# Performance work log

Measured on AMD Instinct MI355X. Metric: run time of the kernel, lower is better.

Reference implementation:

```python
import jax, jax.numpy as jnp
import numpy as np

ALPHA = 1.1
COMMISSION = 0.05
BET_PCT = 0.02
B = 4_194_304
T = 6  # num traps


def setup_inputs() -> dict:
    key = jax.random.key(0)
    k1, k2, k3, k4 = jax.random.split(key, 4)
    predicted_probs = jax.random.uniform(k1, (B, T), dtype=jnp.float32)
    true_winners = (jax.random.uniform(k2, (B, T)) > 0.8).astype(jnp.float32)
    market_odds = jax.random.uniform(k3, (B, T), dtype=jnp.float32) * 10.0
    invalid = jax.random.uniform(k4, (B, 1)) < 0.1
    market_odds = jnp.where(invalid, 0.0, market_odds)
    return {"predicted_probs": predicted_probs, "true_winners": true_winners,
            "market_odds": market_odds}


def reference(predicted_probs, true_winners, market_odds):
    batch_size = predicted_probs.shape[0]
    payout_scale = BET_PCT * (1.0 - COMMISSION)

    has_valid_odds = jnp.any(market_odds > 0, axis=1)  # [B]
    # expected profit per dog; zero for races without valid odds
    ep = (market_odds * ALPHA * predicted_probs - 1.0) * payout_scale  # [B,T]
    ep = jnp.where(has_valid_odds[:, None], ep, 0.0)

    best_idx = jnp.argmax(ep, axis=1)  # [B], first-max like torch
    best_ep = jnp.take_along_axis(ep, best_idx[:, None], axis=1)[:, 0]  # [B]
    should_bet = (best_ep > 0) & has_valid_odds  # [B]

    # actual profits (not part of the differentiable loss; tracked as metrics)
    odds_b = jnp.take_along_axis(market_odds, best_idx[:, None], axis=1)[:, 0]
    win_b = jnp.take_along_axis(true_winners, best_idx[:, None], axis=1)[:, 0]
    win_profit = (odds_b * ALPHA * BET_PCT - BET_PCT) * (1.0 - COMMISSION)
    lose_profit = -BET_PCT * (1.0 - COMMISSION)
    actual_profits = jnp.where(should_bet,
                               jnp.where(win_b > 0.5, win_profit, lose_profit),
                               0.0)

    any_bet = jnp.any(should_bet)
    sum_bet_ep = jnp.sum(jnp.where(should_bet, best_ep, 0.0))
    fallback = -jnp.mean(jnp.max(predicted_probs, axis=1)) * 0.1
    total_expected_profit = jnp.where(any_bet, sum_bet_ep, fallback)
    loss = -total_expected_profit / batch_size

    batch_profit = jnp.sum(actual_profits)
    num_bets = jnp.sum(should_bet.astype(jnp.int32))
    return loss, batch_profit, num_bets
```

## Files before the change

kernel.cpp:

```cpp
#include <hip/hip_runtime.h>
#include <math.h>


constexpr int T = 6;
constexpr int NBLK = 2048;
constexpr int NTHR = 256;

__global__ __launch_bounds__(NTHR) void betting_stage1(
    const float* __restrict__ probs,
    const float* __restrict__ winners,
    const float* __restrict__ odds,
    double* __restrict__ partials,
    int B)
{
    const float ALPHA = 1.1f;
    const float BET = 0.02f;
    const float KEEP = 0.95f;
    const float PS = BET * KEEP;

    double s_ep = 0.0, s_profit = 0.0, s_maxp = 0.0;
    int cnt = 0;

    const int stride = gridDim.x * blockDim.x;
    for (int r = blockIdx.x * blockDim.x + threadIdx.x; r < B; r += stride) {
        const float2* P = (const float2*)probs + (size_t)r * 3;
        const float2* O = (const float2*)odds  + (size_t)r * 3;
        float2 p0 = P[0], p1 = P[1], p2 = P[2];
        float2 o0 = O[0], o1 = O[1], o2 = O[2];
        float p[T] = {p0.x, p0.y, p1.x, p1.y, p2.x, p2.y};
        float o[T] = {o0.x, o0.y, o1.x, o1.y, o2.x, o2.y};

        bool valid = false;
        float maxp = p[0];
        #pragma unroll
        for (int j = 0; j < T; ++j) {
            valid |= (o[j] > 0.0f);
            maxp = fmaxf(maxp, p[j]);
        }
        s_maxp += (double)maxp;

        if (valid) {
            float best_ep = -INFINITY;
            int best = 0;
            #pragma unroll
            for (int j = 0; j < T; ++j) {
                float ep = (o[j] * ALPHA * p[j] - 1.0f) * PS;
                if (ep > best_ep) { best_ep = ep; best = j; }
            }
            if (best_ep > 0.0f) {
                s_ep += (double)best_ep;
                cnt += 1;
                float w = winners[(size_t)r * T + best];
                float ob = o[best];
                float profit = (w > 0.5f)
                    ? (ob * ALPHA * BET - BET) * KEEP
                    : -BET * KEEP;
                s_profit += (double)profit;
            }
        }
    }

    #pragma unroll
    for (int off = 32; off > 0; off >>= 1) {
        s_ep     += __shfl_down(s_ep, off);
        s_profit += __shfl_down(s_profit, off);
        s_maxp   += __shfl_down(s_maxp, off);
        cnt      += __shfl_down(cnt, off);
    }

    __shared__ double sm_ep[NTHR / 64];
    __shared__ double sm_pr[NTHR / 64];
    __shared__ double sm_mx[NTHR / 64];
    __shared__ int    sm_ct[NTHR / 64];
    const int lane = threadIdx.x & 63;
    const int wid  = threadIdx.x >> 6;
    if (lane == 0) {
        sm_ep[wid] = s_ep; sm_pr[wid] = s_profit; sm_mx[wid] = s_maxp; sm_ct[wid] = cnt;
    }
    __syncthreads();
    if (threadIdx.x == 0) {
        double t_ep = 0.0, t_pr = 0.0, t_mx = 0.0; int t_ct = 0;
        #pragma unroll
        for (int i = 0; i < NTHR / 64; ++i) {
            t_ep += sm_ep[i]; t_pr += sm_pr[i]; t_mx += sm_mx[i]; t_ct += sm_ct[i];
        }
        double* slot = partials + (size_t)blockIdx.x * 4;
        slot[0] = t_ep; slot[1] = t_pr; slot[2] = t_mx; slot[3] = (double)t_ct;
    }
}

__global__ __launch_bounds__(NTHR) void betting_stage2(
    const double* __restrict__ partials, float* __restrict__ out, int nblk, int B)
{
    double s_ep = 0.0, s_pr = 0.0, s_mx = 0.0, s_ct = 0.0;
    for (int i = threadIdx.x; i < nblk; i += blockDim.x) {
        const double* slot = partials + (size_t)i * 4;
        s_ep += slot[0]; s_pr += slot[1]; s_mx += slot[2]; s_ct += slot[3];
    }
    #pragma unroll
    for (int off = 32; off > 0; off >>= 1) {
        s_ep += __shfl_down(s_ep, off);
        s_pr += __shfl_down(s_pr, off);
        s_mx += __shfl_down(s_mx, off);
        s_ct += __shfl_down(s_ct, off);
    }
    __shared__ double sm[4][NTHR / 64];
    const int lane = threadIdx.x & 63;
    const int wid  = threadIdx.x >> 6;
    if (lane == 0) { sm[0][wid] = s_ep; sm[1][wid] = s_pr; sm[2][wid] = s_mx; sm[3][wid] = s_ct; }
    __syncthreads();
    if (threadIdx.x == 0) {
        double ep = 0.0, pr = 0.0, mx = 0.0, ct = 0.0;
        #pragma unroll
        for (int i = 0; i < NTHR / 64; ++i) { ep += sm[0][i]; pr += sm[1][i]; mx += sm[2][i]; ct += sm[3][i]; }
        bool any_bet = ct > 0.0;
        double total = any_bet ? ep : (-(mx / (double)B) * 0.1);
        out[0] = (float)(-total / (double)B);
        out[1] = (float)pr;
        out[2] = (float)ct;
    }
}

extern "C" void kernel_launch(void* const* d_in, const int* in_sizes, int n_in,
                              void* d_out, int out_size, void* d_ws, size_t ws_size,
                              hipStream_t stream) {
    const float* probs   = (const float*)d_in[0];
    const float* winners = (const float*)d_in[1];
    const float* odds    = (const float*)d_in[2];
    float* out = (float*)d_out;
    const int B = in_sizes[0] / T;

    double* partials = (double*)d_ws;

    betting_stage1<<<NBLK, NTHR, 0, stream>>>(probs, winners, odds, partials, B);
    betting_stage2<<<1, NTHR, 0, stream>>>(partials, out, NBLK, B);
}
```

Baseline: 278.0 us.

## Process row pairs with float4 loads and stream winners densely

Each thread now handles two races at once, reading probs, odds and winners as three float4 vectors per array instead of float2 loads plus a scattered winner gather. The winner value is carried along during the argmax, so the dependent indexed load goes away and the accumulation becomes branchless. The cost is reading the whole winners array (more bytes than the sparse gather, though gathered 4-byte reads still pulled in whole cache lines). It also assumes B is even, since a trailing odd row would be silently dropped.

```diff
diff --git a/kernel.cpp b/kernel.cpp
--- a/kernel.cpp
+++ b/kernel.cpp
@@ -7,11 +7,11 @@
 constexpr int NTHR = 256;
 
 __global__ __launch_bounds__(NTHR) void betting_stage1(
-    const float* __restrict__ probs,
-    const float* __restrict__ winners,
-    const float* __restrict__ odds,
+    const float4* __restrict__ probs,
+    const float4* __restrict__ winners,
+    const float4* __restrict__ odds,
     double* __restrict__ partials,
-    int B)
+    int npairs)
 {
     const float ALPHA = 1.1f;
     const float BET = 0.02f;
@@ -22,41 +22,45 @@
     int cnt = 0;
 
     const int stride = gridDim.x * blockDim.x;
-    for (int r = blockIdx.x * blockDim.x + threadIdx.x; r < B; r += stride) {
-        const float2* P = (const float2*)probs + (size_t)r * 3;
-        const float2* O = (const float2*)odds  + (size_t)r * 3;
-        float2 p0 = P[0], p1 = P[1], p2 = P[2];
-        float2 o0 = O[0], o1 = O[1], o2 = O[2];
-        float p[T] = {p0.x, p0.y, p1.x, p1.y, p2.x, p2.y};
-        float o[T] = {o0.x, o0.y, o1.x, o1.y, o2.x, o2.y};
+    for (int i = blockIdx.x * blockDim.x + threadIdx.x; i < npairs; i += stride) {
+        const size_t base = (size_t)i * 3;
+        float4 pa = probs[base + 0], pb = probs[base + 1], pc = probs[base + 2];
+        float4 oa = odds [base + 0], ob = odds [base + 1], oc = odds [base + 2];
+        float4 wa = winners[base + 0], wb = winners[base + 1], wc = winners[base + 2];
 
-        bool valid = false;
-        float maxp = p[0];
+        float p[12] = {pa.x, pa.y, pa.z, pa.w, pb.x, pb.y, pb.z, pb.w, pc.x, pc.y, pc.z, pc.w};
+        float o[12] = {oa.x, oa.y, oa.z, oa.w, ob.x, ob.y, ob.z, ob.w, oc.x, oc.y, oc.z, oc.w};
+        float w[12] = {wa.x, wa.y, wa.z, wa.w, wb.x, wb.y, wb.z, wb.w, wc.x, wc.y, wc.z, wc.w};
+
         #pragma unroll
-        for (int j = 0; j < T; ++j) {
-            valid |= (o[j] > 0.0f);
-            maxp = fmaxf(maxp, p[j]);
-        }
-        s_maxp += (double)maxp;
-
-        if (valid) {
+        for (int rr = 0; rr < 2; ++rr) {
+            const int off = rr * T;
+            bool valid = false;
+            float maxp = p[off];
             float best_ep = -INFINITY;
-            int best = 0;
+            float best_odds = 0.0f, best_win = 0.0f;
             #pragma unroll
             for (int j = 0; j < T; ++j) {
-                float ep = (o[j] * ALPHA * p[j] - 1.0f) * PS;
-                if (ep > best_ep) { best_ep = ep; best = j; }
+                const float oj = o[off + j];
+                const float pj = p[off + j];
+                valid |= (oj > 0.0f);
+                maxp = fmaxf(maxp, pj);
+                const float ep = (oj * ALPHA * pj - 1.0f) * PS;
+                if (ep > best_ep) {
+                    best_ep = ep;
+                    best_odds = oj;
+                    best_win = w[off + j];
+                }
             }
-            if (best_ep > 0.0f) {
-                s_ep += (double)best_ep;
-                cnt += 1;
-                float w = winners[(size_t)r * T + best];
-                float ob = o[best];
-                float profit = (w > 0.5f)
-                    ? (ob * ALPHA * BET - BET) * KEEP
-                    : -BET * KEEP;
-                s_profit += (double)profit;
-            }
+            s_maxp += (double)maxp;
+
+            const bool bet = valid && (best_ep > 0.0f);
+            s_ep += bet ? (double)best_ep : 0.0;
+            cnt += bet ? 1 : 0;
+            const float profit = (best_win > 0.5f)
+                ? (best_odds * ALPHA * BET - BET) * KEEP
+                : -BET * KEEP;
+            s_profit += bet ? (double)profit : 0.0;
         }
     }
 
@@ -129,9 +133,11 @@
     const float* odds    = (const float*)d_in[2];
     float* out = (float*)d_out;
     const int B = in_sizes[0] / T;
+    const int npairs = B / 2;
 
     double* partials = (double*)d_ws;
 
-    betting_stage1<<<NBLK, NTHR, 0, stream>>>(probs, winners, odds, partials, B);
+    betting_stage1<<<NBLK, NTHR, 0, stream>>>(
+        (const float4*)probs, (const float4*)winners, (const float4*)odds, partials, npairs);
     betting_stage2<<<1, NTHR, 0, stream>>>(partials, out, NBLK, B);
 }
```

Result: no change. 281.5 us (+1.3%).
